# Kernel optimization log

Measured on AMD Instinct MI355X. Metric: run time of the kernel, lower is better.

## Reference

```python
import jax, jax.numpy as jnp
import numpy as np

EPSILON = 1e-06
N_TOKENS = 65536
WIDTH_IN = 1024
WIDTH_OUT = 1024
NUM_HEAD = 16
DIM_HEAD = 64


def setup_inputs() -> dict:
    key = jax.random.key(0)
    k_x, k_b, k_lin, k_ker = jax.random.split(key, 4)
    x = jax.random.normal(k_x, (N_TOKENS, WIDTH_IN), dtype=jnp.float32)
    norm_bias = jax.random.normal(k_b, (N_TOKENS, NUM_HEAD, DIM_HEAD), dtype=jnp.float32)
    # LinearLayer: std = 1/sqrt(width_in), shape (width_in, num_head*dim_head)
    w_lin = jax.random.normal(k_lin, (WIDTH_IN, NUM_HEAD * DIM_HEAD), dtype=jnp.float32) / np.sqrt(WIDTH_IN)
    # Grouped kernel: (num_head, dim_head, width_out // num_head), scaled 1/sqrt(dim_head)
    kernel = jax.random.normal(k_ker, (NUM_HEAD, DIM_HEAD, WIDTH_OUT // NUM_HEAD), dtype=jnp.float32) / np.sqrt(DIM_HEAD)
    return {"x": x, "norm_bias": norm_bias, "w_lin": w_lin, "kernel": kernel}


def reference(x, norm_bias, w_lin, kernel):
    # Dense projection, bias-free
    xx = x @ w_lin                                   # [N, H*D]
    xx = xx.reshape(*x.shape[:-1], NUM_HEAD, DIM_HEAD)  # [N, H, D]
    # Per-head RMSNorm
    xx = xx / jnp.sqrt(jnp.mean(jnp.square(xx), axis=-1, keepdims=True) + EPSILON)
    # Optional norm-bias blend
    xx = (xx + norm_bias.reshape(xx.shape)) / 2 ** 0.5
    # Per-head grouped matmul
    xx = jnp.einsum('nhd,hdf->nhf', xx, kernel)      # [N, H, F]
    return xx.reshape(*x.shape[:-1], -1)             # [N, H*F]
```

## Files before the change

kernel.cpp:

```cpp
#include <hip/hip_runtime.h>


typedef __attribute__((ext_vector_type(8))) __bf16 bf16x8;
typedef __attribute__((ext_vector_type(4))) float f32x4;
typedef __attribute__((ext_vector_type(2))) unsigned int uint2v;
typedef __attribute__((ext_vector_type(8))) unsigned short ushort8;

__device__ __forceinline__ unsigned short f2bf(float f) {
  unsigned int u = __builtin_bit_cast(unsigned int, f);
  u += 0x7FFFu + ((u >> 16) & 1u);
  return (unsigned short)(u >> 16);
}

__device__ __forceinline__ f32x4 mfma_bf16(bf16x8 a, bf16x8 b, f32x4 c) {
  return __builtin_amdgcn_mfma_f32_16x16x32_bf16(a, b, c, 0, 0, 0);
}

__device__ __forceinline__ void gl_lds16(const void* g, void* l) {
  __builtin_amdgcn_global_load_lds(
      (const __attribute__((address_space(1))) unsigned int*)g,
      (__attribute__((address_space(3))) unsigned int*)l, 16, 0, 0);
}

__global__ void prep_w2(const float* __restrict__ w, unsigned short* __restrict__ wb) {
  const int kt = blockIdx.x, ct = blockIdx.y, col = threadIdx.x;
  #pragma unroll
  for (int kc = 0; kc < 8; ++kc) {
    ushort8 v;
    #pragma unroll
    for (int j = 0; j < 8; ++j) {
      const int k = kt * 64 + (kc >> 2) * 32 + (kc & 3) * 8 + j;
      v[j] = f2bf(w[(size_t)k * 1024 + ct * 128 + col]);
    }
    *reinterpret_cast<ushort8*>(wb + ((((size_t)ct * 16 + kt) * 8 + kc) * 128 + col) * 8) = v;
  }
}

__global__ void transpose_k(const float* __restrict__ kin, unsigned short* __restrict__ kt) {
  __shared__ float tile[64][65];
  const int h = blockIdx.x;
  const int t = threadIdx.x;
  #pragma unroll
  for (int i = 0; i < 16; ++i) {
    int idx = i * 256 + t;
    tile[idx >> 6][idx & 63] = kin[(size_t)h * 4096 + idx];
  }
  __syncthreads();
  #pragma unroll
  for (int i = 0; i < 16; ++i) {
    int idx = i * 256 + t;
    kt[(size_t)h * 4096 + idx] = f2bf(tile[idx & 63][idx >> 6]);
  }
}

__global__ __launch_bounds__(256, 2)
void fused_main(const float* __restrict__ x,
                const float* __restrict__ nbias,
                const unsigned short* __restrict__ wb,
                const unsigned short* __restrict__ ktg,
                float* __restrict__ out)
{
  __shared__ __align__(16) unsigned char smem[65536];
  const int tid = threadIdx.x;
  const int wv = tid >> 6, lane = tid & 63, l15 = lane & 15, lg = lane >> 4;
  const int wr = wv >> 1, wc = wv & 1;
  const int bid = blockIdx.x;
  const int gx = bid & 7, slot = bid >> 3;
  const int rt = ((slot >> 3) << 3) + gx;
  const int ct = slot & 7;
  const size_t row0 = (size_t)rt * 128;

  const float* xb = x + row0 * 1024;
  const unsigned char* wsrc = reinterpret_cast<const unsigned char*>(wb) + (size_t)ct * 262144;

  const int ar_ = tid >> 4, ac_ = tid & 15;
  const float* agp = xb + (size_t)ar_ * 1024 + ac_ * 4;
  const int aw_off = (ac_ * 8) ^ ((ar_ & 7) << 4);

  const int abase = (wr * 64 + l15) * 128;
  const int aswz  = (l15 & 7) << 4;
  const int ofs0  = (lg * 16) ^ aswz;
  const int ofs1  = (64 + lg * 16) ^ aswz;
  const int bcol  = (wc * 64 + l15) * 16 + lg * 2048;

  f32x4 acc[4][4];
  const f32x4 z4 = {0.f, 0.f, 0.f, 0.f};
  #pragma unroll
  for (int mi = 0; mi < 4; ++mi)
    #pragma unroll
    for (int ni = 0; ni < 4; ++ni) acc[mi][ni] = z4;

  f32x4 arg[2][8];

  auto stageB = [&](int t, int bsel) {
    unsigned char* Bb = smem + 32768 + (bsel << 14);
    #pragma unroll
    for (int it = 0; it < 4; ++it) {
      const int L = it * 4096 + tid * 16;
      gl_lds16(wsrc + (size_t)t * 16384 + L, Bb + L);
    }
  };
  auto loadA = [&](int t, f32x4* dst) {
    #pragma unroll
    for (int j = 0; j < 8; ++j)
      dst[j] = *reinterpret_cast<const f32x4*>(agp + j * 16384 + t * 64);
  };
  auto cvtwrA = [&](const f32x4* src, int bsel) {
    unsigned char* Ab = smem + (bsel << 14);
    #pragma unroll
    for (int j = 0; j < 8; ++j) {
      const f32x4 v = src[j];
      unsigned int lo = ((unsigned)__builtin_bit_cast(unsigned short, (__bf16)v[0])) |
                        ((unsigned)__builtin_bit_cast(unsigned short, (__bf16)v[1]) << 16);
      unsigned int hi = ((unsigned)__builtin_bit_cast(unsigned short, (__bf16)v[2])) |
                        ((unsigned)__builtin_bit_cast(unsigned short, (__bf16)v[3]) << 16);
      uint2v p; p[0] = lo; p[1] = hi;
      *reinterpret_cast<uint2v*>(Ab + j * 2048 + ar_ * 128 + aw_off) = p;
    }
  };
  auto phase = [&](int csel, int ks) {
    const unsigned char* Ab = smem + (csel << 14);
    const unsigned char* Bb = smem + 32768 + (csel << 14);
    const int aofs = ks ? ofs1 : ofs0;
    bf16x8 af[4], bq[4];
    #pragma unroll
    for (int mi = 0; mi < 4; ++mi)
      af[mi] = *reinterpret_cast<const bf16x8*>(Ab + abase + mi * 2048 + aofs);
    #pragma unroll
    for (int ni = 0; ni < 4; ++ni)
      bq[ni] = *reinterpret_cast<const bf16x8*>(Bb + (ks << 13) + bcol + ni * 256);
    #pragma unroll
    for (int mi = 0; mi < 4; ++mi)
      #pragma unroll
      for (int ni = 0; ni < 4; ++ni)
        acc[mi][ni] = mfma_bf16(af[mi], bq[ni], acc[mi][ni]);
  };

  stageB(0, 0);
  __builtin_amdgcn_sched_barrier(0);
  loadA(0, arg[0]);
  loadA(1, arg[1]);
  __builtin_amdgcn_sched_barrier(0);
  cvtwrA(arg[0], 0);
  asm volatile("s_waitcnt lgkmcnt(0)" ::: "memory");
  __builtin_amdgcn_sched_barrier(0);
  __builtin_amdgcn_s_barrier();
  __builtin_amdgcn_sched_barrier(0);

  #pragma unroll
  for (int t = 0; t < 16; ++t) {
    const int c = t & 1, n = c ^ 1;
    if (t + 1 < 16) stageB(t + 1, n);
    __builtin_amdgcn_sched_barrier(0);
    if (t + 2 < 16) loadA(t + 2, arg[c]);
    __builtin_amdgcn_sched_barrier(0);

    phase(c, 0);
    if (t + 1 < 16) cvtwrA(arg[n], n);
    phase(c, 1);

    if (t + 1 < 16) {
      asm volatile("s_waitcnt lgkmcnt(0)" ::: "memory");
      if (t + 2 < 16) asm volatile("s_waitcnt vmcnt(8)" ::: "memory");
      else            asm volatile("s_waitcnt vmcnt(0)" ::: "memory");
      __builtin_amdgcn_sched_barrier(0);
      __builtin_amdgcn_s_barrier();
      __builtin_amdgcn_sched_barrier(0);
    }
  }

  __syncthreads();

  const int h = ct * 2 + wc;
  unsigned short* yw = reinterpret_cast<unsigned short*>(smem) + wv * 4096;
  const float* bb = nbias + (row0 + wr * 64) * 1024 + (size_t)h * 64 + l15;

  #pragma unroll
  for (int mi = 0; mi < 4; ++mi) {
    float ss[4];
    #pragma unroll
    for (int r = 0; r < 4; ++r) {
      float p = 0.f;
      #pragma unroll
      for (int ni = 0; ni < 4; ++ni) { const float v = acc[mi][ni][r]; p += v * v; }
      ss[r] = p;
    }
    #pragma unroll
    for (int s = 1; s < 16; s <<= 1)
      #pragma unroll
      for (int r = 0; r < 4; ++r) ss[r] += __shfl_xor(ss[r], s, 64);
    #pragma unroll
    for (int r = 0; r < 4; ++r) {
      const float rs = rsqrtf(ss[r] * 0.015625f + 1e-6f);
      const int rl = mi * 16 + lg * 4 + r;
      const float* bp = bb + (size_t)rl * 1024;
      #pragma unroll
      for (int ni = 0; ni < 4; ++ni) {
        const float y = (acc[mi][ni][r] * rs + bp[ni * 16]) * 0.70710678118654752f;
        const __bf16 yb = (__bf16)y;
        yw[rl * 64 + ((ni * 16 + l15) ^ ((rl & 7) << 3))] = __builtin_bit_cast(unsigned short, yb);
      }
    }
  }

  const unsigned short* ktp = ktg + (size_t)h * 4096;
  bf16x8 b2[4][2];
  #pragma unroll
  for (int ff = 0; ff < 4; ++ff)
    #pragma unroll
    for (int ks = 0; ks < 2; ++ks)
      b2[ff][ks] = *reinterpret_cast<const bf16x8*>(ktp + (ff * 16 + l15) * 64 + ks * 32 + 8 * lg);

  #pragma unroll
  for (int m2 = 0; m2 < 4; ++m2) {
    f32x4 a2[4] = {z4, z4, z4, z4};
    const int row = m2 * 16 + l15;
    #pragma unroll
    for (int ks = 0; ks < 2; ++ks) {
      bf16x8 a = *reinterpret_cast<const bf16x8*>(
          yw + row * 64 + ((ks * 32 + lg * 8) ^ ((row & 7) << 3)));
      #pragma unroll
      for (int ff = 0; ff < 4; ++ff) a2[ff] = mfma_bf16(a, b2[ff][ks], a2[ff]);
    }
    float* ob = out + (row0 + wr * 64 + m2 * 16 + lg * 4) * 1024 + ct * 128 + wc * 64 + l15;
    #pragma unroll
    for (int ff = 0; ff < 4; ++ff)
      #pragma unroll
      for (int r = 0; r < 4; ++r)
        ob[(size_t)r * 1024 + ff * 16] = a2[ff][r];
  }
}

extern "C" void kernel_launch(void* const* d_in, const int* in_sizes, int n_in,
                              void* d_out, int out_size, void* d_ws, size_t ws_size,
                              hipStream_t stream) {
  const float* x  = (const float*)d_in[0];
  const float* nb = (const float*)d_in[1];
  const float* wl = (const float*)d_in[2];
  const float* kr = (const float*)d_in[3];
  float* out = (float*)d_out;

  unsigned short* wbp = (unsigned short*)d_ws;
  unsigned short* ktp = wbp + 1024 * 1024;

  hipLaunchKernelGGL(prep_w2, dim3(16, 8), dim3(128), 0, stream, wl, wbp);
  hipLaunchKernelGGL(transpose_k, dim3(16), dim3(256), 0, stream, kr, ktp);
  hipLaunchKernelGGL(fused_main, dim3(4096), dim3(256), 0, stream, x, nb, wbp, ktp, out);
}
```

Baseline: 301.4 us.

## Halve K-tile to 32, shrink LDS to 32KB, raise occupancy to three blocks

```diff
diff --git a/kernel.cpp b/kernel.cpp
--- a/kernel.cpp
+++ b/kernel.cpp
@@ -3,19 +3,14 @@
 
 typedef __attribute__((ext_vector_type(8))) __bf16 bf16x8;
 typedef __attribute__((ext_vector_type(4))) float f32x4;
-typedef __attribute__((ext_vector_type(2))) unsigned int uint2v;
 typedef __attribute__((ext_vector_type(8))) unsigned short ushort8;
 
-__device__ __forceinline__ unsigned short f2bf(float f) {
-  unsigned int u = __builtin_bit_cast(unsigned int, f);
-  u += 0x7FFFu + ((u >> 16) & 1u);
-  return (unsigned short)(u >> 16);
-}
-
+__device__ __forceinline__ unsigned short bfbits(float f) {
+  return __builtin_bit_cast(unsigned short, (__bf16)f);
+}
 __device__ __forceinline__ f32x4 mfma_bf16(bf16x8 a, bf16x8 b, f32x4 c) {
   return __builtin_amdgcn_mfma_f32_16x16x32_bf16(a, b, c, 0, 0, 0);
 }
-
 __device__ __forceinline__ void gl_lds16(const void* g, void* l) {
   __builtin_amdgcn_global_load_lds(
       (const __attribute__((address_space(1))) unsigned int*)g,
@@ -23,16 +18,14 @@
 }
 
 __global__ void prep_w2(const float* __restrict__ w, unsigned short* __restrict__ wb) {
-  const int kt = blockIdx.x, ct = blockIdx.y, col = threadIdx.x;
-  #pragma unroll
-  for (int kc = 0; kc < 8; ++kc) {
+  const int t = blockIdx.x, ct = blockIdx.y, col = threadIdx.x;
+  #pragma unroll
+  for (int kc = 0; kc < 4; ++kc) {
     ushort8 v;
     #pragma unroll
-    for (int j = 0; j < 8; ++j) {
-      const int k = kt * 64 + (kc >> 2) * 32 + (kc & 3) * 8 + j;
-      v[j] = f2bf(w[(size_t)k * 1024 + ct * 128 + col]);
-    }
-    *reinterpret_cast<ushort8*>(wb + ((((size_t)ct * 16 + kt) * 8 + kc) * 128 + col) * 8) = v;
+    for (int j = 0; j < 8; ++j)
+      v[j] = bfbits(w[(size_t)(t * 32 + kc * 8 + j) * 1024 + ct * 128 + col]);
+    *reinterpret_cast<ushort8*>(wb + (((size_t)(ct * 32 + t) * 4 + kc) * 128 + col) * 8) = v;
   }
 }
 
@@ -49,39 +42,34 @@
   #pragma unroll
   for (int i = 0; i < 16; ++i) {
     int idx = i * 256 + t;
-    kt[(size_t)h * 4096 + idx] = f2bf(tile[idx & 63][idx >> 6]);
-  }
-}
-
-__global__ __launch_bounds__(256, 2)
+    kt[(size_t)h * 4096 + idx] = bfbits(tile[idx & 63][idx >> 6]);
+  }
+}
+
+__global__ __launch_bounds__(256, 3)
 void fused_main(const float* __restrict__ x,
                 const float* __restrict__ nbias,
                 const unsigned short* __restrict__ wb,
                 const unsigned short* __restrict__ ktg,
                 float* __restrict__ out)
 {
-  __shared__ __align__(16) unsigned char smem[65536];
+  __shared__ __align__(16) unsigned char smem[32768];
   const int tid = threadIdx.x;
   const int wv = tid >> 6, lane = tid & 63, l15 = lane & 15, lg = lane >> 4;
   const int wr = wv >> 1, wc = wv & 1;
   const int bid = blockIdx.x;
   const int gx = bid & 7, slot = bid >> 3;
-  const int rt = ((slot >> 3) << 3) + gx;
-  const int ct = slot & 7;
+  const int v = gx * 512 + slot;
+  const int rt = v >> 3, ct = v & 7;
   const size_t row0 = (size_t)rt * 128;
 
-  const float* xb = x + row0 * 1024;
-  const unsigned char* wsrc = reinterpret_cast<const unsigned char*>(wb) + (size_t)ct * 262144;
-
-  const int ar_ = tid >> 4, ac_ = tid & 15;
-  const float* agp = xb + (size_t)ar_ * 1024 + ac_ * 4;
-  const int aw_off = (ac_ * 8) ^ ((ar_ & 7) << 4);
-
-  const int abase = (wr * 64 + l15) * 128;
-  const int aswz  = (l15 & 7) << 4;
-  const int ofs0  = (lg * 16) ^ aswz;
-  const int ofs1  = (64 + lg * 16) ^ aswz;
-  const int bcol  = (wc * 64 + l15) * 16 + lg * 2048;
+  const int sr = tid >> 1, sh = tid & 1;
+  const float* agp = x + (row0 + sr) * 1024 + sh * 16;
+  const unsigned char* wsrc =
+      reinterpret_cast<const unsigned char*>(wb) + (size_t)ct * 262144;
+
+  const int aoff = lg * 2048 + (wr * 64 + l15) * 16;
+  const int boff = lg * 2048 + (wc * 64 + l15) * 16;
 
   f32x4 acc[4][4];
   const f32x4 z4 = {0.f, 0.f, 0.f, 0.f};
@@ -90,54 +78,49 @@
     #pragma unroll
     for (int ni = 0; ni < 4; ++ni) acc[mi][ni] = z4;
 
-  f32x4 arg[2][8];
+  f32x4 arg[2][4];
 
   auto stageB = [&](int t, int bsel) {
-    unsigned char* Bb = smem + 32768 + (bsel << 14);
-    #pragma unroll
-    for (int it = 0; it < 4; ++it) {
-      const int L = it * 4096 + tid * 16;
-      gl_lds16(wsrc + (size_t)t * 16384 + L, Bb + L);
-    }
+    unsigned char* Bb = smem + 16384 + (bsel << 13);
+    const unsigned char* bs = wsrc + (size_t)t * 8192;
+    gl_lds16(bs + tid * 16,        Bb + tid * 16);
+    gl_lds16(bs + 4096 + tid * 16, Bb + 4096 + tid * 16);
   };
   auto loadA = [&](int t, f32x4* dst) {
-    #pragma unroll
-    for (int j = 0; j < 8; ++j)
-      dst[j] = *reinterpret_cast<const f32x4*>(agp + j * 16384 + t * 64);
+    const float* p = agp + t * 32;
+    #pragma unroll
+    for (int j = 0; j < 4; ++j) dst[j] = *reinterpret_cast<const f32x4*>(p + j * 4);
   };
   auto cvtwrA = [&](const f32x4* src, int bsel) {
-    unsigned char* Ab = smem + (bsel << 14);
-    #pragma unroll
-    for (int j = 0; j < 8; ++j) {
-      const f32x4 v = src[j];
-      unsigned int lo = ((unsigned)__builtin_bit_cast(unsigned short, (__bf16)v[0])) |
-                        ((unsigned)__builtin_bit_cast(unsigned short, (__bf16)v[1]) << 16);
-      unsigned int hi = ((unsigned)__builtin_bit_cast(unsigned short, (__bf16)v[2])) |
-                        ((unsigned)__builtin_bit_cast(unsigned short, (__bf16)v[3]) << 16);
-      uint2v p; p[0] = lo; p[1] = hi;
-      *reinterpret_cast<uint2v*>(Ab + j * 2048 + ar_ * 128 + aw_off) = p;
-    }
-  };
-  auto phase = [&](int csel, int ks) {
-    const unsigned char* Ab = smem + (csel << 14);
-    const unsigned char* Bb = smem + 32768 + (csel << 14);
-    const int aofs = ks ? ofs1 : ofs0;
+    unsigned char* Ab = smem + (bsel << 13);
+    ushort8 v0, v1;
+    #pragma unroll
+    for (int j = 0; j < 4; ++j) { v0[j] = bfbits(src[0][j]); v0[4 + j] = bfbits(src[1][j]); }
+    #pragma unroll
+    for (int j = 0; j < 4; ++j) { v1[j] = bfbits(src[2][j]); v1[4 + j] = bfbits(src[3][j]); }
+    *reinterpret_cast<ushort8*>(Ab + (2 * sh) * 2048 + sr * 16)     = v0;
+    *reinterpret_cast<ushort8*>(Ab + (2 * sh + 1) * 2048 + sr * 16) = v1;
+  };
+  auto compute = [&](int csel) {
+    const unsigned char* Ab = smem + (csel << 13);
+    const unsigned char* Bb = smem + 16384 + (csel << 13);
     bf16x8 af[4], bq[4];
     #pragma unroll
     for (int mi = 0; mi < 4; ++mi)
-      af[mi] = *reinterpret_cast<const bf16x8*>(Ab + abase + mi * 2048 + aofs);
+      af[mi] = *reinterpret_cast<const bf16x8*>(Ab + aoff + mi * 256);
     #pragma unroll
     for (int ni = 0; ni < 4; ++ni)
-      bq[ni] = *reinterpret_cast<const bf16x8*>(Bb + (ks << 13) + bcol + ni * 256);
+      bq[ni] = *reinterpret_cast<const bf16x8*>(Bb + boff + ni * 256);
+    __builtin_amdgcn_s_setprio(1);
     #pragma unroll
     for (int mi = 0; mi < 4; ++mi)
       #pragma unroll
       for (int ni = 0; ni < 4; ++ni)
         acc[mi][ni] = mfma_bf16(af[mi], bq[ni], acc[mi][ni]);
+    __builtin_amdgcn_s_setprio(0);
   };
 
   stageB(0, 0);
-  __builtin_amdgcn_sched_barrier(0);
   loadA(0, arg[0]);
   loadA(1, arg[1]);
   __builtin_amdgcn_sched_barrier(0);
@@ -148,27 +131,24 @@
   __builtin_amdgcn_sched_barrier(0);
 
   #pragma unroll
-  for (int t = 0; t < 16; ++t) {
+  for (int t = 0; t < 32; ++t) {
     const int c = t & 1, n = c ^ 1;
-    if (t + 1 < 16) stageB(t + 1, n);
-    __builtin_amdgcn_sched_barrier(0);
-    if (t + 2 < 16) loadA(t + 2, arg[c]);
-    __builtin_amdgcn_sched_barrier(0);
-
-    phase(c, 0);
-    if (t + 1 < 16) cvtwrA(arg[n], n);
-    phase(c, 1);
-
-    if (t + 1 < 16) {
+    if (t + 1 < 32) { stageB(t + 1, n); __builtin_amdgcn_sched_barrier(0); }
+    if (t + 2 < 32) { loadA(t + 2, arg[c]); __builtin_amdgcn_sched_barrier(0); }
+
+    compute(c);
+    if (t + 1 < 32) cvtwrA(arg[n], n);
+
+    if (t + 1 < 32) {
       asm volatile("s_waitcnt lgkmcnt(0)" ::: "memory");
-      if (t + 2 < 16) asm volatile("s_waitcnt vmcnt(8)" ::: "memory");
+      if (t + 2 < 32) asm volatile("s_waitcnt vmcnt(4)" ::: "memory");
       else            asm volatile("s_waitcnt vmcnt(0)" ::: "memory");
       __builtin_amdgcn_sched_barrier(0);
       __builtin_amdgcn_s_barrier();
       __builtin_amdgcn_sched_barrier(0);
     }
   }
-
+  __builtin_amdgcn_sched_barrier(0);
   __syncthreads();
 
   const int h = ct * 2 + wc;
@@ -182,7 +162,7 @@
     for (int r = 0; r < 4; ++r) {
       float p = 0.f;
       #pragma unroll
-      for (int ni = 0; ni < 4; ++ni) { const float v = acc[mi][ni][r]; p += v * v; }
+      for (int ni = 0; ni < 4; ++ni) { const float q = acc[mi][ni][r]; p += q * q; }
       ss[r] = p;
     }
     #pragma unroll
@@ -197,8 +177,7 @@
       #pragma unroll
       for (int ni = 0; ni < 4; ++ni) {
         const float y = (acc[mi][ni][r] * rs + bp[ni * 16]) * 0.70710678118654752f;
-        const __bf16 yb = (__bf16)y;
-        yw[rl * 64 + ((ni * 16 + l15) ^ ((rl & 7) << 3))] = __builtin_bit_cast(unsigned short, yb);
+        yw[rl * 64 + ((ni * 16 + l15) ^ ((rl & 7) << 3))] = bfbits(y);
       }
     }
   }
@@ -209,7 +188,7 @@
   for (int ff = 0; ff < 4; ++ff)
     #pragma unroll
     for (int ks = 0; ks < 2; ++ks)
-      b2[ff][ks] = *reinterpret_cast<const bf16x8*>(ktp + (ff * 16 + l15) * 64 + ks * 32 + 8 * lg);
+      b2[ff][ks] = *reinterpret_cast<const bf16x8*>(ktp + (ff * 16 + l15) * 64 + ks * 32 + lg * 8);
 
   #pragma unroll
   for (int m2 = 0; m2 < 4; ++m2) {
@@ -241,9 +220,9 @@
   float* out = (float*)d_out;
 
   unsigned short* wbp = (unsigned short*)d_ws;
-  unsigned short* ktp = wbp + 1024 * 1024;
-
-  hipLaunchKernelGGL(prep_w2, dim3(16, 8), dim3(128), 0, stream, wl, wbp);
+  unsigned short* ktp = wbp + 1048576;
+
+  hipLaunchKernelGGL(prep_w2, dim3(32, 8), dim3(128), 0, stream, wl, wbp);
   hipLaunchKernelGGL(transpose_k, dim3(16), dim3(256), 0, stream, kr, ktp);
   hipLaunchKernelGGL(fused_main, dim3(4096), dim3(256), 0, stream, x, nb, wbp, ktp, out);
 }
```

Result: slower. 330.5 us (+9.6%).
